# Optimization experiments

Measured on AMD Instinct MI355X. Metric: run time of the kernel, lower is better.

The kernel has to match this reference:

```python
import jax, jax.numpy as jnp
from jax import lax
import numpy as np

K = 2000      # self.k: entries kept per sample
T_SC = 3      # number of IHT iterations
DN = ('NCHW', 'OIHW', 'NCHW')


def keep_k_largest(X, k):
    # Per-sample hard threshold: keep the k largest-magnitude entries of the
    # flattened [C,H,W] activations, zero the rest (exactly k kept, as in argsort).
    B = X.shape[0]
    flat = X.reshape(B, -1)                                # [B, N]
    _, idx = lax.top_k(jnp.abs(flat), k)                   # [B, k]
    vals = jnp.take_along_axis(flat, idx, axis=1)          # [B, k]
    out = jnp.zeros_like(flat).at[jnp.arange(B)[:, None], idx].set(vals)
    return out.reshape(X.shape)


def _D_apply(X, W_D):
    # ConvTranspose2d(numb_atom -> dp_channels), stride 1, no padding:
    # full correlation with the spatially flipped, io-swapped kernel.
    kh, kw = W_D.shape[2], W_D.shape[3]
    Wt = jnp.flip(jnp.transpose(W_D, (1, 0, 2, 3)), (2, 3))  # [dp, atoms, kh, kw]
    return lax.conv_general_dilated(X, Wt, (1, 1),
                                    [(kh - 1, kh - 1), (kw - 1, kw - 1)],
                                    dimension_numbers=DN)


def _Dt_apply(Z, W_D):
    # Conv2d(dp_channels -> numb_atom) VALID; D_trans.weight = D.weight.permute(0,1,3,2)
    Wt = jnp.transpose(W_D, (0, 1, 3, 2))                  # [atoms, dp, kh, kw]
    return lax.conv_general_dilated(Z, Wt, (1, 1), 'VALID', dimension_numbers=DN)


def setup_inputs() -> dict:
    key = jax.random.key(0)
    k1, k2, k3 = jax.random.split(key, 3)
    Y = jax.random.normal(k1, (32, 3, 64, 64), jnp.float32)
    X0 = jax.random.normal(k2, (32, 128, 57, 57), jnp.float32)   # random init X in forward
    W_D = jax.random.normal(k3, (128, 3, 8, 8), jnp.float32) * 0.05
    return {"Y": Y, "X0": X0, "W_D": W_D}


def reference(Y, X0, W_D):
    # HT_arg = X - D_trans(D(X) - Y); then T_SC hard-threshold iterations.
    HT_arg = X0 - _Dt_apply(_D_apply(X0, W_D) - Y, W_D)
    X = HT_arg
    for i in range(T_SC):
        X = keep_k_largest(HT_arg, K)
        if i < T_SC - 1:  # final HT_arg update in the original is unused
            HT_arg = X - _Dt_apply(_D_apply(X, W_D) - Y, W_D)
    return X
```

## Files before the change

### kernel.cpp

```cpp
#include <hip/hip_runtime.h>

#define BATCH 32
#define ATOMS 128
#define CCH 3
#define XH 57
#define XW 57
#define OHH 64
#define OWW 64
#define KSEL 2000
#define PIX (XH*XW)
#define NPS (ATOMS*PIX)
#define NTOT (BATCH*NPS)
#define RPS (CCH*OHH*OWW)
#define RTOT (BATCH*RPS)
#define CANDCAP 32768
#define NW 24576
#define WSEG 102

__global__ __launch_bounds__(256) void wprep_k(const float* __restrict__ Wg,
    double* __restrict__ WDd, double* __restrict__ Wt2d) {
  int e = blockIdx.x * 256 + threadIdx.x;
  if (e >= NW) return;
  {
    int kw = e & 7; int t = e >> 3; int c = t % 3; t /= 3; int kh = t & 7; int a = t >> 3;
    WDd[e] = (double)Wg[(a*3 + c)*64 + kh*8 + kw];
  }
  {
    int a = e & 127; int t = e >> 7; int j = t & 7; int i = (t >> 3) & 7; int c = t >> 6;
    Wt2d[e] = (double)Wg[(a*3 + c)*64 + j*8 + i];
  }
}

__global__ __launch_bounds__(256) void rinit_k(const float* __restrict__ Y,
    double* __restrict__ Rd) {
  int i = blockIdx.x * 256 + threadIdx.x;
  if (i < RTOT) Rd[i] = -(double)Y[i];
}

__global__ __launch_bounds__(256) void rfin_k(const double* __restrict__ Rd,
    float* __restrict__ R) {
  int i = blockIdx.x * 256 + threadIdx.x;
  if (i < RTOT) R[i] = (float)Rd[i];
}

__global__ __launch_bounds__(256) void convD_k(const float* __restrict__ X,
    const double* __restrict__ WDd, double* __restrict__ Rd) {
  __shared__ float Xs[8][9][72];
  int p = blockIdx.x;
  int lg = (p & 7) * 256 + (p >> 3);
  int b = lg >> 6; int rem = lg & 63;
  int band = rem >> 1, half = rem & 1;
  int oy0 = band * 2;
  int a_base = half * 64;
  int tid = threadIdx.x;
  int ox = tid & 63;
  int wv = __builtin_amdgcn_readfirstlane(tid >> 6);
  const float* Xb = X + (size_t)b * NPS;

  double acc[2][3];
#pragma unroll
  for (int ty = 0; ty < 2; ++ty)
#pragma unroll
    for (int c = 0; c < 3; ++c) acc[ty][c] = 0.0;

  for (int ch = 0; ch < 8; ++ch) {
    __syncthreads();
    for (int e = tid; e < 8 * 9 * 72; e += 256) {
      int ai = e / 648; int rem2 = e - ai * 648;
      int r = rem2 / 72; int ss = rem2 - r * 72;
      int gy = oy0 - 7 + r;
      int xcol = ss - 7;
      int a = a_base + ch * 8 + ai;
      float v = 0.0f;
      if ((unsigned)xcol < (unsigned)XW && (unsigned)gy < (unsigned)XH)
        v = Xb[a * PIX + gy * XW + xcol];
      Xs[ai][r][ss] = v;
    }
    __syncthreads();
#pragma unroll
    for (int jj = 0; jj < 2; ++jj) {
      int ai = (wv << 1) + jj;
      int a  = a_base + ch * 8 + ai;
      const double* Wa = WDd + a * 192;
      for (int r = 0; r < 9; ++r) {
        int gy = oy0 - 7 + r;
        if ((unsigned)gy >= (unsigned)XH) continue;
        double xd[8];
#pragma unroll
        for (int t = 0; t < 8; ++t) xd[t] = (double)Xs[ai][r][ox + t];
        if (r <= 7) {
          const double* Wk = Wa + (7 - r) * 24;
#pragma unroll
          for (int kw = 0; kw < 8; ++kw) {
            acc[0][0] = fma(xd[7 - kw], Wk[kw],      acc[0][0]);
            acc[0][1] = fma(xd[7 - kw], Wk[8 + kw],  acc[0][1]);
            acc[0][2] = fma(xd[7 - kw], Wk[16 + kw], acc[0][2]);
          }
        }
        if (r >= 1) {
          const double* Wk = Wa + (8 - r) * 24;
#pragma unroll
          for (int kw = 0; kw < 8; ++kw) {
            acc[1][0] = fma(xd[7 - kw], Wk[kw],      acc[1][0]);
            acc[1][1] = fma(xd[7 - kw], Wk[8 + kw],  acc[1][1]);
            acc[1][2] = fma(xd[7 - kw], Wk[16 + kw], acc[1][2]);
          }
        }
      }
    }
  }
#pragma unroll
  for (int ty = 0; ty < 2; ++ty) {
    int oy = oy0 + ty;
#pragma unroll
    for (int c = 0; c < 3; ++c)
      atomicAdd(&Rd[((size_t)(b * CCH + c) << 12) + (oy << 6) + ox], acc[ty][c]);
  }
}

__global__ __launch_bounds__(256) void convD_sparse_k(const float* __restrict__ Wg,
    const int* __restrict__ nzidx, const float* __restrict__ nzval,
    const float* __restrict__ Y, float* __restrict__ R) {
  __shared__ double accd[512];
  __shared__ float Wf[8192];
  __shared__ int   li[KSEL];
  __shared__ float lv[KSEL];
  int p = blockIdx.x;
  int lg = (p & 7) * 96 + (p >> 3);
  int s = lg / 24; int r = lg % 24; int c = r >> 3; int band = r & 7;
  int row0 = band * 8;
  int tid = threadIdx.x;
  for (int e = tid; e < 512; e += 256) accd[e] = 0.0;
  for (int e = tid; e < 8192; e += 256) {
    int a = e >> 6, k2 = e & 63;
    Wf[e] = Wg[(a * 3 + c) * 64 + k2];
  }
  for (int e = tid; e < KSEL; e += 256) {
    li[e] = nzidx[s * KSEL + e];
    lv[e] = nzval[s * KSEL + e];
  }
  __syncthreads();
  int slot = tid >> 3, kw = tid & 7;
  for (int e = slot; e < KSEL; e += 32) {
    int idx = li[e];
    int a = (int)((unsigned)idx / 3249u);
    int pp = idx - a * 3249;
    int y = (int)((unsigned)pp / 57u);
    int x = pp - y * 57;
    int dy = y - row0;
    if (dy < -7 || dy > 7) continue;
    double val = (double)lv[e];
    const float* wp = Wf + (a << 6) + kw;
#pragma unroll
    for (int kh = 0; kh < 8; ++kh) {
      int rr = dy + kh;
      if ((unsigned)rr < 8u)
        __hip_atomic_fetch_add(&accd[(rr << 6) + x + kw],
                               val * (double)wp[kh << 3],
                               __ATOMIC_RELAXED, __HIP_MEMORY_SCOPE_WORKGROUP);
    }
  }
  __syncthreads();
  const float* Yb = Y + (((size_t)(s * CCH + c)) << 12) + (row0 << 6);
  float* Rb = R + (((size_t)(s * CCH + c)) << 12) + (row0 << 6);
  for (int e = tid; e < 512; e += 256)
    Rb[e] = (float)(accd[e] - (double)Yb[e]);
}

__global__ __launch_bounds__(256) void convDt_k(const float* __restrict__ R,
    const double* __restrict__ Wt2d, const float* __restrict__ Xprev,
    float* __restrict__ HT, unsigned* __restrict__ g1) {
  __shared__ float Rl[3][15][72];
  __shared__ unsigned hh[1024];
  int p = blockIdx.x;
  int lg = (p & 7) * 512 + (p >> 3);
  int b = lg >> 7; int rem = lg & 127; int ag = rem >> 3; int by = rem & 7;
  int row0 = by * 8;
  int a0 = ag * 8;
  int tid = threadIdx.x;
  for (int e = tid; e < 1024; e += 256) hh[e] = 0;
  for (int e = tid; e < 3 * 15 * 72; e += 256) {
    int c = e / (15 * 72); int r2 = e - c * (15 * 72);
    int rr = r2 / 72; int cc = r2 - rr * 72;
    int gr = row0 + rr;
    float v = 0.0f;
    if (cc < OWW && gr < OHH)
      v = R[((size_t)(b * CCH + c) << 12) + (gr << 6) + cc];
    Rl[c][rr][cc] = v;
  }
  __syncthreads();
  int x = tid & 63, yg = tid >> 6;
  int yb = yg * 2;
  double acc[8][2];
#pragma unroll
  for (int aa = 0; aa < 8; ++aa) { acc[aa][0] = 0.0; acc[aa][1] = 0.0; }

#pragma unroll 1
  for (int c = 0; c < 3; ++c) {
#pragma unroll 1
    for (int j = 0; j < 8; ++j) {
      double rw[9];
#pragma unroll
      for (int r = 0; r < 9; ++r) rw[r] = (double)Rl[c][yb + r][x + j];
#pragma unroll
      for (int i = 0; i < 8; ++i) {
        const double* wp = Wt2d + ((c * 8 + i) * 8 + j) * 128 + a0;
#pragma unroll
        for (int aa = 0; aa < 8; ++aa) {
          double w = wp[aa];
          acc[aa][0] = fma(rw[i + 0], w, acc[aa][0]);
          acc[aa][1] = fma(rw[i + 1], w, acc[aa][1]);
        }
      }
    }
  }
  if (x < XW) {
#pragma unroll
    for (int ty = 0; ty < 2; ++ty) {
      int yy = row0 + yb + ty;
      if (yy < XH) {
#pragma unroll
        for (int aa = 0; aa < 8; ++aa) {
          size_t xo = (size_t)(b * ATOMS + a0 + aa) * PIX + yy * XW + x;
          float fv = (float)((double)Xprev[xo] - acc[aa][ty]);
          HT[xo] = fv;
          unsigned u = __float_as_uint(fv) & 0x7fffffffu;
          unsigned bin = u >> 20;
          atomicAdd(&hh[bin >> 1], 1u << ((bin & 1) << 4));
        }
      }
    }
  }
  __syncthreads();
  unsigned* gp = g1 + (size_t)b * 2048;
  for (int e = tid; e < 1024; e += 256) {
    unsigned v = hh[e];
    unsigned lo = v & 0xffffu, hi = v >> 16;
    if (lo) atomicAdd(&gp[2 * e], lo);
    if (hi) atomicAdd(&gp[2 * e + 1], hi);
  }
}

template <int NB>
__global__ __launch_bounds__(256) void find_k(const unsigned* __restrict__ gh,
    const int* __restrict__ Kin, int* __restrict__ Bout, int* __restrict__ Kout) {
  int s = blockIdx.x;
  const unsigned* h = gh + s * NB;
  __shared__ unsigned part[256];
  constexpr int C = NB / 256;
  int t = threadIdx.x;
  unsigned sum = 0;
#pragma unroll
  for (int e = 0; e < C; ++e) sum += h[t * C + e];
  part[t] = sum;
  __syncthreads();
  if (t == 0) {
    int Kv = Kin ? Kin[s] : KSEL;
    unsigned cumBefore = 0;
    int bsel = 0;
    for (int q = 255; q >= 0; --q) {
      unsigned ps = part[q];
      if ((int)(cumBefore + ps) >= Kv) {
        for (int e = q * C + C - 1;; --e) {
          unsigned c2 = cumBefore + h[e];
          if ((int)c2 >= Kv) { bsel = e; break; }
          cumBefore = c2;
        }
        break;
      }
      cumBefore += ps;
    }
    Bout[s] = bsel;
    Kout[s] = Kv - (int)cumBefore;
  }
}

__global__ __launch_bounds__(256) void hist2_k(const float* __restrict__ HT,
    const int* __restrict__ b1, unsigned* __restrict__ g2,
    int* __restrict__ cand, int* __restrict__ candcnt) {
  __shared__ unsigned h[1024];
  __shared__ int lidx[4096];
  __shared__ int lcnt, lbase;
  for (int e = threadIdx.x; e < 1024; e += 256) h[e] = 0;
  if (threadIdx.x == 0) lcnt = 0;
  __syncthreads();
  int s = blockIdx.x >> 5;
  int chunk = blockIdx.x & 31;
  unsigned pre = (unsigned)b1[s];
  const uint4* U4 = (const uint4*)(HT + (size_t)s * NPS);
  for (int i4 = chunk * 256 + threadIdx.x; i4 < NPS / 4; i4 += 32 * 256) {
    uint4 v = U4[i4];
    unsigned uu[4] = {v.x, v.y, v.z, v.w};
#pragma unroll
    for (int t = 0; t < 4; ++t) {
      unsigned u = uu[t] & 0x7fffffffu;
      if ((u >> 20) == pre) {
        atomicAdd(&h[(u >> 10) & 1023], 1u);
        int pos = atomicAdd(&lcnt, 1);
        if (pos < 4096) lidx[pos] = i4 * 4 + t;
      }
    }
  }
  __syncthreads();
  if (threadIdx.x == 0) {
    int n = lcnt < 4096 ? lcnt : 4096;
    lbase = atomicAdd(&candcnt[s], n);
  }
  __syncthreads();
  int n = lcnt < 4096 ? lcnt : 4096;
  int base = lbase;
  for (int e = threadIdx.x; e < n; e += 256) {
    int g = base + e;
    if (g < CANDCAP) cand[s * CANDCAP + g] = lidx[e];
  }
  for (int e = threadIdx.x; e < 1024; e += 256)
    if (h[e]) atomicAdd(&g2[s * 1024 + e], h[e]);
}

__global__ __launch_bounds__(256) void pass3_k(const float* __restrict__ HT,
    const int* __restrict__ cand, const int* __restrict__ candcnt,
    const int* __restrict__ b1, const unsigned* __restrict__ g2,
    const int* __restrict__ k1, unsigned* __restrict__ tau_out,
    int* __restrict__ cutoff_out) {
  int s = blockIdx.x;
  __shared__ unsigned h[1024];
  __shared__ unsigned part[256];
  __shared__ int eqidx[1024];
  __shared__ int eqn;
  __shared__ unsigned tau_sh;
  __shared__ int k3_sh;
  __shared__ int b2_sh, k2_sh;
  int t = threadIdx.x;
  const unsigned* hg = g2 + s * 1024;
  unsigned sum = 0;
#pragma unroll
  for (int e = 0; e < 4; ++e) sum += hg[t * 4 + e];
  part[t] = sum;
  for (int e = t; e < 1024; e += 256) h[e] = 0;
  if (t == 0) eqn = 0;
  __syncthreads();
  if (t == 0) {
    int Kv = k1[s];
    unsigned cumBefore = 0;
    int bsel = 0;
    for (int q = 255; q >= 0; --q) {
      unsigned ps = part[q];
      if ((int)(cumBefore + ps) >= Kv) {
        for (int e = q * 4 + 3;; --e) {
          unsigned c2 = cumBefore + hg[e];
          if ((int)c2 >= Kv) { bsel = e; break; }
          cumBefore = c2;
        }
        break;
      }
      cumBefore += ps;
    }
    b2_sh = bsel;
    k2_sh = Kv - (int)cumBefore;
  }
  __syncthreads();
  int n = candcnt[s];
  if (n > CANDCAP) n = CANDCAP;
  unsigned pre21 = (((unsigned)b1[s]) << 10) | (unsigned)b2_sh;
  const unsigned* U = (const unsigned*)(HT + (size_t)s * NPS);
  for (int e = t; e < n; e += 256) {
    int i = cand[s * CANDCAP + e];
    unsigned u = U[i] & 0x7fffffffu;
    if ((u >> 10) == pre21) atomicAdd(&h[u & 1023], 1u);
  }
  __syncthreads();
  if (t == 0) {
    int Kv = k2_sh;
    unsigned cumBefore = 0;
    int b3 = 0;
    for (int e = 1023; e >= 0; --e) {
      unsigned c2 = cumBefore + h[e];
      if ((int)c2 >= Kv) { b3 = e; break; }
      cumBefore = c2;
    }
    tau_sh = (pre21 << 10) | (unsigned)b3;
    k3_sh = Kv - (int)cumBefore;
  }
  __syncthreads();
  unsigned tau = tau_sh;
  for (int e = t; e < n; e += 256) {
    int i = cand[s * CANDCAP + e];
    unsigned u = U[i] & 0x7fffffffu;
    if (u == tau) {
      int pos = atomicAdd(&eqn, 1);
      if (pos < 1024) eqidx[pos] = i;
    }
  }
  __syncthreads();
  if (t == 0) {
    int m = eqn < 1024 ? eqn : 1024;
    int k3 = k3_sh;
    int cutoff;
    if (k3 >= m) {
      cutoff = 0x7fffffff;
    } else {
      int last = -1;
      for (int r = 0; r < k3; ++r) {
        int mn = 0x7fffffff;
        for (int q = 0; q < m; ++q) {
          int v = eqidx[q];
          if (v > last && v < mn) mn = v;
        }
        last = mn;
      }
      cutoff = last;
    }
    tau_out[s] = tau;
    cutoff_out[s] = cutoff;
  }
}

__global__ __launch_bounds__(256) void write_k(const float* __restrict__ HT,
    const unsigned* __restrict__ tau, const int* __restrict__ cutoff,
    float* __restrict__ Xo, int* __restrict__ nzidx, float* __restrict__ nzval,
    int* __restrict__ nzcnt) {
  __shared__ int lidx[2048];
  __shared__ float lval[2048];
  __shared__ int lcnt, lbase;
  int s = blockIdx.x / WSEG;
  int seg = blockIdx.x % WSEG;
  int tid = threadIdx.x;
  if (tid == 0) lcnt = 0;
  __syncthreads();
  unsigned tt = tau[s];
  int co = cutoff[s];
  size_t sbase = (size_t)s * NPS;
  const float4* H4 = (const float4*)(HT + sbase);
  float4* X4 = (float4*)(Xo + sbase);
  int f0 = seg * 1024;
#pragma unroll
  for (int rr = 0; rr < 4; ++rr) {
    int i4 = f0 + rr * 256 + tid;
    if (i4 < NPS / 4) {
      float4 v = H4[i4];
      float vv[4] = {v.x, v.y, v.z, v.w};
      float oo[4];
#pragma unroll
      for (int t = 0; t < 4; ++t) {
        int il = i4 * 4 + t;
        unsigned u = __float_as_uint(vv[t]) & 0x7fffffffu;
        bool keep = (u > tt) || (u == tt && il <= co);
        oo[t] = keep ? vv[t] : 0.0f;
        if (keep) {
          int pos = atomicAdd(&lcnt, 1);
          if (pos < 2048) { lidx[pos] = il; lval[pos] = vv[t]; }
        }
      }
      X4[i4] = make_float4(oo[0], oo[1], oo[2], oo[3]);
    }
  }
  __syncthreads();
  if (tid == 0) lbase = atomicAdd(&nzcnt[s], lcnt);
  __syncthreads();
  int n = lcnt < 2048 ? lcnt : 2048;
  int base = lbase;
  for (int e = tid; e < n; e += 256) {
    int g = base + e;
    if (g < KSEL) { nzidx[s * KSEL + g] = lidx[e]; nzval[s * KSEL + g] = lval[e]; }
  }
}

extern "C" void kernel_launch(void* const* d_in, const int* in_sizes, int n_in,
                              void* d_out, int out_size, void* d_ws, size_t ws_size,
                              hipStream_t stream) {
  const float* Y  = (const float*)d_in[0];
  const float* X0 = (const float*)d_in[1];
  const float* Wg = (const float*)d_in[2];
  float* Xout = (float*)d_out;

  double* WDd  = (double*)d_ws;
  double* Wt2d = WDd + NW;
  float* HT   = (float*)(Wt2d + NW);
  float* Rbuf = HT + NTOT;
  double* Rd  = (double*)(Rbuf + RTOT);
  unsigned* g1 = (unsigned*)(Rd + RTOT);
  unsigned* g2 = g1 + 32 * 2048;
  int* candcnt = (int*)(g2 + 32 * 1024);
  int* nzcnt = candcnt + 32;
  int* b1 = nzcnt + 32;
  int* k1 = b1 + 32;
  unsigned* tau = (unsigned*)(k1 + 32);
  int* cutoff = (int*)(tau + 32);
  int* cand = cutoff + 32;
  int* nzidx = cand + 32 * CANDCAP;
  float* nzval = (float*)(nzidx + 32 * KSEL);
  size_t zero_bytes = (size_t)(32 * 2048 + 32 * 1024 + 32 + 32) * 4;

  wprep_k<<<dim3((NW + 255) / 256), dim3(256), 0, stream>>>(Wg, WDd, Wt2d);

  for (int it = 0; it < 3; ++it) {
    const float* Xsrc = (it == 0) ? X0 : (const float*)Xout;
    hipMemsetAsync(g1, 0, zero_bytes, stream);
    if (it == 0) {
      rinit_k<<<dim3((RTOT + 255) / 256), dim3(256), 0, stream>>>(Y, Rd);
      convD_k<<<dim3(2048), dim3(256), 0, stream>>>(Xsrc, WDd, Rd);
      rfin_k<<<dim3((RTOT + 255) / 256), dim3(256), 0, stream>>>(Rd, Rbuf);
    } else {
      convD_sparse_k<<<dim3(BATCH * CCH * 8), dim3(256), 0, stream>>>(
          Wg, nzidx, nzval, Y, Rbuf);
    }
    convDt_k<<<dim3(4096), dim3(256), 0, stream>>>(Rbuf, Wt2d, Xsrc, HT, g1);
    find_k<2048><<<dim3(BATCH), dim3(256), 0, stream>>>(g1, (const int*)nullptr, b1, k1);
    hist2_k<<<dim3(BATCH * 32), dim3(256), 0, stream>>>(HT, b1, g2, cand, candcnt);
    pass3_k<<<dim3(BATCH), dim3(256), 0, stream>>>(HT, cand, candcnt, b1, g2, k1, tau, cutoff);
    write_k<<<dim3(BATCH * WSEG), dim3(256), 0, stream>>>(HT, tau, cutoff, Xout,
                                                          nzidx, nzval, nzcnt);
  }
}
```

Measured before the change: 1.078 ms.

## Fuse prep kernels, retile dense transposed conv, skip final sparse list emission

Merges the weight-prep and residual-init kernels into one launch, and drops the double-to-float conversion kernel by templating convDt_k to read the double residual directly. The dense convD kernel now covers 4 output rows and 32 atoms per block instead of 2 rows and 64 atoms. This reuses each staged input row across more output rows, at the cost of more accumulators and a larger shared tile. The last iteration's write kernel no longer builds the nonzero index/value list, since nothing reads it afterwards.

```diff
diff --git a/kernel.cpp b/kernel.cpp
--- a/kernel.cpp
+++ b/kernel.cpp
@@ -17,58 +17,49 @@
 #define NW 24576
 #define WSEG 102
 
-__global__ __launch_bounds__(256) void wprep_k(const float* __restrict__ Wg,
-    double* __restrict__ WDd, double* __restrict__ Wt2d) {
+__global__ __launch_bounds__(256) void prep_k(const float* __restrict__ Wg,
+    double* __restrict__ WDd, double* __restrict__ Wt2d,
+    const float* __restrict__ Y, double* __restrict__ Rd) {
   int e = blockIdx.x * 256 + threadIdx.x;
-  if (e >= NW) return;
-  {
-    int kw = e & 7; int t = e >> 3; int c = t % 3; t /= 3; int kh = t & 7; int a = t >> 3;
-    WDd[e] = (double)Wg[(a*3 + c)*64 + kh*8 + kw];
-  }
-  {
-    int a = e & 127; int t = e >> 7; int j = t & 7; int i = (t >> 3) & 7; int c = t >> 6;
-    Wt2d[e] = (double)Wg[(a*3 + c)*64 + j*8 + i];
-  }
-}
-
-__global__ __launch_bounds__(256) void rinit_k(const float* __restrict__ Y,
-    double* __restrict__ Rd) {
-  int i = blockIdx.x * 256 + threadIdx.x;
-  if (i < RTOT) Rd[i] = -(double)Y[i];
-}
-
-__global__ __launch_bounds__(256) void rfin_k(const double* __restrict__ Rd,
-    float* __restrict__ R) {
-  int i = blockIdx.x * 256 + threadIdx.x;
-  if (i < RTOT) R[i] = (float)Rd[i];
+  if (e < NW) {
+    {
+      int kw = e & 7; int t = e >> 3; int c = t % 3; t /= 3; int kh = t & 7; int a = t >> 3;
+      WDd[e] = (double)Wg[(a*3 + c)*64 + kh*8 + kw];
+    }
+    {
+      int a = e & 127; int t = e >> 7; int j = t & 7; int i = (t >> 3) & 7; int c = t >> 6;
+      Wt2d[e] = (double)Wg[(a*3 + c)*64 + j*8 + i];
+    }
+  }
+  if (e < RTOT) Rd[e] = -(double)Y[e];
 }
 
 __global__ __launch_bounds__(256) void convD_k(const float* __restrict__ X,
     const double* __restrict__ WDd, double* __restrict__ Rd) {
-  __shared__ float Xs[8][9][72];
+  __shared__ float Xs[8][11][72];
   int p = blockIdx.x;
   int lg = (p & 7) * 256 + (p >> 3);
   int b = lg >> 6; int rem = lg & 63;
-  int band = rem >> 1, half = rem & 1;
-  int oy0 = band * 2;
-  int a_base = half * 64;
+  int band = rem >> 2, quarter = rem & 3;
+  int row0 = band * 4;
+  int a_base = quarter * 32;
   int tid = threadIdx.x;
   int ox = tid & 63;
   int wv = __builtin_amdgcn_readfirstlane(tid >> 6);
   const float* Xb = X + (size_t)b * NPS;
 
-  double acc[2][3];
-#pragma unroll
-  for (int ty = 0; ty < 2; ++ty)
+  double acc[4][3];
+#pragma unroll
+  for (int ty = 0; ty < 4; ++ty)
 #pragma unroll
     for (int c = 0; c < 3; ++c) acc[ty][c] = 0.0;
 
-  for (int ch = 0; ch < 8; ++ch) {
+  for (int ch = 0; ch < 4; ++ch) {
     __syncthreads();
-    for (int e = tid; e < 8 * 9 * 72; e += 256) {
-      int ai = e / 648; int rem2 = e - ai * 648;
+    for (int e = tid; e < 8 * 11 * 72; e += 256) {
+      int ai = e / 792; int rem2 = e - ai * 792;
       int r = rem2 / 72; int ss = rem2 - r * 72;
-      int gy = oy0 - 7 + r;
+      int gy = row0 - 7 + r;
       int xcol = ss - 7;
       int a = a_base + ch * 8 + ai;
       float v = 0.0f;
@@ -82,36 +73,32 @@
       int ai = (wv << 1) + jj;
       int a  = a_base + ch * 8 + ai;
       const double* Wa = WDd + a * 192;
-      for (int r = 0; r < 9; ++r) {
-        int gy = oy0 - 7 + r;
+#pragma unroll
+      for (int r = 0; r < 11; ++r) {
+        int gy = row0 - 7 + r;
         if ((unsigned)gy >= (unsigned)XH) continue;
         double xd[8];
 #pragma unroll
         for (int t = 0; t < 8; ++t) xd[t] = (double)Xs[ai][r][ox + t];
-        if (r <= 7) {
-          const double* Wk = Wa + (7 - r) * 24;
-#pragma unroll
-          for (int kw = 0; kw < 8; ++kw) {
-            acc[0][0] = fma(xd[7 - kw], Wk[kw],      acc[0][0]);
-            acc[0][1] = fma(xd[7 - kw], Wk[8 + kw],  acc[0][1]);
-            acc[0][2] = fma(xd[7 - kw], Wk[16 + kw], acc[0][2]);
+#pragma unroll
+        for (int ty = 0; ty < 4; ++ty) {
+          int kh = ty + 7 - r;
+          if ((unsigned)kh < 8u) {
+            const double* Wk = Wa + kh * 24;
+#pragma unroll
+            for (int kw = 0; kw < 8; ++kw) {
+              acc[ty][0] = fma(xd[7 - kw], Wk[kw],      acc[ty][0]);
+              acc[ty][1] = fma(xd[7 - kw], Wk[8 + kw],  acc[ty][1]);
+              acc[ty][2] = fma(xd[7 - kw], Wk[16 + kw], acc[ty][2]);
+            }
           }
         }
-        if (r >= 1) {
-          const double* Wk = Wa + (8 - r) * 24;
-#pragma unroll
-          for (int kw = 0; kw < 8; ++kw) {
-            acc[1][0] = fma(xd[7 - kw], Wk[kw],      acc[1][0]);
-            acc[1][1] = fma(xd[7 - kw], Wk[8 + kw],  acc[1][1]);
-            acc[1][2] = fma(xd[7 - kw], Wk[16 + kw], acc[1][2]);
-          }
-        }
-      }
-    }
-  }
-#pragma unroll
-  for (int ty = 0; ty < 2; ++ty) {
-    int oy = oy0 + ty;
+      }
+    }
+  }
+#pragma unroll
+  for (int ty = 0; ty < 4; ++ty) {
+    int oy = row0 + ty;
 #pragma unroll
     for (int c = 0; c < 3; ++c)
       atomicAdd(&Rd[((size_t)(b * CCH + c) << 12) + (oy << 6) + ox], acc[ty][c]);
@@ -167,7 +154,8 @@
     Rb[e] = (float)(accd[e] - (double)Yb[e]);
 }
 
-__global__ __launch_bounds__(256) void convDt_k(const float* __restrict__ R,
+template <typename TR>
+__global__ __launch_bounds__(256) void convDt_k(const TR* __restrict__ R,
     const double* __restrict__ Wt2d, const float* __restrict__ Xprev,
     float* __restrict__ HT, unsigned* __restrict__ g1) {
   __shared__ float Rl[3][15][72];
@@ -185,7 +173,7 @@
     int gr = row0 + rr;
     float v = 0.0f;
     if (cc < OWW && gr < OHH)
-      v = R[((size_t)(b * CCH + c) << 12) + (gr << 6) + cc];
+      v = (float)R[((size_t)(b * CCH + c) << 12) + (gr << 6) + cc];
     Rl[c][rr][cc] = v;
   }
   __syncthreads();
@@ -425,6 +413,7 @@
   int s = blockIdx.x / WSEG;
   int seg = blockIdx.x % WSEG;
   int tid = threadIdx.x;
+  bool emit = (nzidx != nullptr);
   if (tid == 0) lcnt = 0;
   __syncthreads();
   unsigned tt = tau[s];
@@ -446,7 +435,7 @@
         unsigned u = __float_as_uint(vv[t]) & 0x7fffffffu;
         bool keep = (u > tt) || (u == tt && il <= co);
         oo[t] = keep ? vv[t] : 0.0f;
-        if (keep) {
+        if (keep && emit) {
           int pos = atomicAdd(&lcnt, 1);
           if (pos < 2048) { lidx[pos] = il; lval[pos] = vv[t]; }
         }
@@ -454,6 +443,7 @@
       X4[i4] = make_float4(oo[0], oo[1], oo[2], oo[3]);
     }
   }
+  if (!emit) return;
   __syncthreads();
   if (tid == 0) lbase = atomicAdd(&nzcnt[s], lcnt);
   __syncthreads();
@@ -491,24 +481,24 @@
   float* nzval = (float*)(nzidx + 32 * KSEL);
   size_t zero_bytes = (size_t)(32 * 2048 + 32 * 1024 + 32 + 32) * 4;
 
-  wprep_k<<<dim3((NW + 255) / 256), dim3(256), 0, stream>>>(Wg, WDd, Wt2d);
+  prep_k<<<dim3((RTOT + 255) / 256), dim3(256), 0, stream>>>(Wg, WDd, Wt2d, Y, Rd);
 
   for (int it = 0; it < 3; ++it) {
     const float* Xsrc = (it == 0) ? X0 : (const float*)Xout;
     hipMemsetAsync(g1, 0, zero_bytes, stream);
     if (it == 0) {
-      rinit_k<<<dim3((RTOT + 255) / 256), dim3(256), 0, stream>>>(Y, Rd);
       convD_k<<<dim3(2048), dim3(256), 0, stream>>>(Xsrc, WDd, Rd);
-      rfin_k<<<dim3((RTOT + 255) / 256), dim3(256), 0, stream>>>(Rd, Rbuf);
+      convDt_k<double><<<dim3(4096), dim3(256), 0, stream>>>(Rd, Wt2d, Xsrc, HT, g1);
     } else {
       convD_sparse_k<<<dim3(BATCH * CCH * 8), dim3(256), 0, stream>>>(
           Wg, nzidx, nzval, Y, Rbuf);
-    }
-    convDt_k<<<dim3(4096), dim3(256), 0, stream>>>(Rbuf, Wt2d, Xsrc, HT, g1);
+      convDt_k<float><<<dim3(4096), dim3(256), 0, stream>>>(Rbuf, Wt2d, Xsrc, HT, g1);
+    }
     find_k<2048><<<dim3(BATCH), dim3(256), 0, stream>>>(g1, (const int*)nullptr, b1, k1);
     hist2_k<<<dim3(BATCH * 32), dim3(256), 0, stream>>>(HT, b1, g2, cand, candcnt);
     pass3_k<<<dim3(BATCH), dim3(256), 0, stream>>>(HT, cand, candcnt, b1, g2, k1, tau, cutoff);
+    bool last = (it == 2);
     write_k<<<dim3(BATCH * WSEG), dim3(256), 0, stream>>>(HT, tau, cutoff, Xout,
-                                                          nzidx, nzval, nzcnt);
-  }
-}
+        last ? nullptr : nzidx, last ? nullptr : nzval, nzcnt);
+  }
+}
```

Result: faster. 1.006 ms (-6.7%).
